# Kernel optimization log

Hardware: AMD Instinct MI355X
Metric: run time of the kernel (lower is better)

The kernel has to match this reference:

```python
import jax, jax.numpy as jnp
import numpy as np

B, N, FIN, E, OUT, NH = 8, 1024, 128, 128, 128, 8
HD = E // NH  # head_dim = 16


def setup_inputs() -> dict:
    key = jax.random.key(0)
    ks = jax.random.split(key, 8)
    s = 0.05
    H = jax.random.normal(ks[0], (B, N, FIN), jnp.float32)
    # binary adjacency (sparse-ish graph), stored dense float as the module expects
    A = (jax.random.uniform(ks[1], (B, N, N)) < 0.05).astype(jnp.float32)
    W_lin = jax.random.normal(ks[2], (FIN, E), jnp.float32) * s
    b_lin = jnp.zeros((E,), jnp.float32)
    # nn.MultiheadAttention packed in-projection (q,k,v) and out-projection
    W_in = jax.random.normal(ks[3], (E, 3 * E), jnp.float32) * s
    b_in = jnp.zeros((3 * E,), jnp.float32)
    W_out = jax.random.normal(ks[4], (E, E), jnp.float32) * s
    b_out = jnp.zeros((E,), jnp.float32)
    W_fin = jax.random.normal(ks[5], (E, OUT), jnp.float32) * s
    b_fin = jnp.zeros((OUT,), jnp.float32)
    return dict(H=H, A=A, W_lin=W_lin, b_lin=b_lin, W_in=W_in, b_in=b_in,
                W_out=W_out, b_out=b_out, W_fin=W_fin, b_fin=b_fin)


def reference(H, A, W_lin, b_lin, W_in, b_in, W_out, b_out, W_fin, b_fin):
    # input projection: Linear(128, embed_dim)
    Hp = H @ W_lin + b_lin                                   # (B,N,E)
    # adjacency-gated attention weights: bmm -> LeakyReLU(0.2) -> *A -> softmax
    s = jnp.einsum('bnd,bmd->bnm', Hp, Hp)                   # (B,N,N)
    s = jnp.where(s >= 0, s, 0.2 * s)
    attn_w = jax.nn.softmax(s * A, axis=-1)                  # (B,N,N)
    # nn.MultiheadAttention self-attention with float attn_mask (ADDED to scores)
    qkv = Hp @ W_in + b_in                                   # (B,N,3E)
    q, k, v = jnp.split(qkv, 3, axis=-1)
    q = q.reshape(B, N, NH, HD)
    k = k.reshape(B, N, NH, HD)
    v = v.reshape(B, N, NH, HD)
    scores = jnp.einsum('bnhd,bmhd->bhnm', q, k) / np.sqrt(HD).astype(np.float32)
    scores = scores + attn_w[:, None]                        # mask broadcast over heads
    p = jax.nn.softmax(scores, axis=-1)                      # (B,NH,N,N)
    o = jnp.einsum('bhnm,bmhd->bnhd', p, v).reshape(B, N, E)
    o = o @ W_out + b_out                                    # MHA out_proj
    # output linear; dropout is identity in eval mode
    return o @ W_fin + b_fin                                 # (B,N,OUT)
```

## Files before the change

kernel.cpp:

```cpp
#include <hip/hip_runtime.h>
#include <hip/hip_bf16.h>


using u16 = unsigned short;
typedef short bf16x8 __attribute__((ext_vector_type(8)));
typedef float f32x4 __attribute__((ext_vector_type(4)));
typedef _Float16 f16;
typedef _Float16 f16x4 __attribute__((ext_vector_type(4)));

#define MFMA16(a, b, c) __builtin_amdgcn_mfma_f32_16x16x16f16(a, b, c, 0, 0, 0)

__device__ __forceinline__ u16 f2b(float f) {
    unsigned u = __float_as_uint(f);
    return (u16)((u + 0x7fffu + ((u >> 16) & 1u)) >> 16);
}
__device__ __forceinline__ float b2f(u16 u) {
    return __uint_as_float(((unsigned)u) << 16);
}

__global__ void prep_hp(const float* __restrict__ H, const float* __restrict__ Wlin,
                        const float* __restrict__ Win,
                        const float* __restrict__ Wout, const float* __restrict__ Wfin,
                        const float* __restrict__ bout, const float* __restrict__ bfin,
                        const float* __restrict__ blin, const float* __restrict__ Aadj,
                        u16* __restrict__ WinTb, u16* __restrict__ WcombTb,
                        float* __restrict__ bcomb, float* __restrict__ rowsum,
                        unsigned char* __restrict__ A8, u16* __restrict__ Hpb) {
    if (blockIdx.x < 64) {
        const int m0 = blockIdx.x * 128;
        const int t = threadIdx.x;
        const int wave = t >> 6, lane = t & 63;
        const int wm = (wave >> 1) * 64, wn = (wave & 1) * 64;
        const int m16 = lane & 15, kq = lane >> 4;
        f32x4 acc[4][4] = {};

#pragma unroll
        for (int kc = 0; kc < 4; ++kc) {
            bf16x8 af[4], bf[4];
#pragma unroll
            for (int i = 0; i < 4; ++i) {
                const float* ap = &H[(long long)(m0 + wm + i * 16 + m16) * 128 + kc * 32 + kq * 8];
                float4 u0 = *(const float4*)ap;
                float4 u1 = *(const float4*)(ap + 4);
                bf16x8 a;
                a[0] = (short)f2b(u0.x); a[1] = (short)f2b(u0.y);
                a[2] = (short)f2b(u0.z); a[3] = (short)f2b(u0.w);
                a[4] = (short)f2b(u1.x); a[5] = (short)f2b(u1.y);
                a[6] = (short)f2b(u1.z); a[7] = (short)f2b(u1.w);
                af[i] = a;
            }
#pragma unroll
            for (int j = 0; j < 4; ++j) {
                const int col = wn + j * 16 + m16;
                const int k0 = kc * 32 + kq * 8;
                bf16x8 bb;
#pragma unroll
                for (int e = 0; e < 8; ++e)
                    bb[e] = (short)f2b(Wlin[(long long)(k0 + e) * 128 + col]);
                bf[j] = bb;
            }
#pragma unroll
            for (int i = 0; i < 4; ++i)
#pragma unroll
                for (int j = 0; j < 4; ++j)
                    acc[i][j] = __builtin_amdgcn_mfma_f32_16x16x32_bf16(af[i], bf[j], acc[i][j], 0, 0, 0);
        }
#pragma unroll
        for (int i = 0; i < 4; ++i) {
#pragma unroll
            for (int r = 0; r < 4; ++r) {
                long long row = m0 + wm + i * 16 + kq * 4 + r;
#pragma unroll
                for (int j = 0; j < 4; ++j) {
                    int col = wn + j * 16 + m16;
                    Hpb[row * 128 + col] = f2b(acc[i][j][r] + blin[col]);
                }
            }
        }
        return;
    }
    int i = (blockIdx.x - 64) * 256 + threadIdx.x;
    if (i >= 81920) {
        int j = i - 81920;
        long long base = (long long)j * 8;
        float4 a0 = *(const float4*)&Aadj[base];
        float4 a1 = *(const float4*)&Aadj[base + 4];
        unsigned long long m = 0;
        m |= (unsigned long long)(a0.x != 0.f) << 0;
        m |= (unsigned long long)(a0.y != 0.f) << 8;
        m |= (unsigned long long)(a0.z != 0.f) << 16;
        m |= (unsigned long long)(a0.w != 0.f) << 24;
        m |= (unsigned long long)(a1.x != 0.f) << 32;
        m |= (unsigned long long)(a1.y != 0.f) << 40;
        m |= (unsigned long long)(a1.z != 0.f) << 48;
        m |= (unsigned long long)(a1.w != 0.f) << 56;
        *(unsigned long long*)&A8[base] = m;
        return;
    }
    if (i < 8192) rowsum[i] = 0.f;
    if (i >= 16384 && i < 65536) {
        int k = i - 16384;
        int r = k / 384, c = k - r * 384;
        WinTb[c * 128 + r] = f2b(Win[k]);
    } else if (i >= 65536) {
        int k = i - 65536;
        int o = k & 127, e = k >> 7;
        float s = 0.f;
        for (int kk = 0; kk < 128; ++kk)
            s = fmaf(Wout[e * 128 + kk], Wfin[kk * 128 + o], s);
        WcombTb[o * 128 + e] = f2b(s);
        if (e == 0) {
            float sb = bfin[o];
            for (int kk = 0; kk < 128; ++kk)
                sb = fmaf(bout[kk], Wfin[kk * 128 + o], sb);
            bcomb[o] = sb;
        }
    }
}

__global__ __launch_bounds__(256)
void mfma_qkvz(const u16* __restrict__ Hpb, const u16* __restrict__ WinTb,
               const float* __restrict__ bin, f16* __restrict__ Cq,
               const unsigned char* __restrict__ G8, u16* __restrict__ EZ,
               float* __restrict__ rowsum) {
    const int blk = blockIdx.x;
    const int t = threadIdx.x;
    const int wave = t >> 6, lane = t & 63;
    const int wm = (wave >> 1) * 64, wn = (wave & 1) * 64;
    const int m16 = lane & 15, kq = lane >> 4;
    f32x4 acc[4][4] = {};

    if (blk < 512) {
        const int b = blk >> 6, mt = (blk >> 3) & 7, nt = blk & 7;
        const u16* Ab = Hpb + (long long)b * 1024 * 128;
        const int m0 = mt * 128, n0 = nt * 128;
#pragma unroll
        for (int kc = 0; kc < 4; ++kc) {
            bf16x8 af[4], bf[4];
#pragma unroll
            for (int i = 0; i < 4; ++i)
                af[i] = *(const bf16x8*)&Ab[(long long)(m0 + wm + i * 16 + m16) * 128 + kc * 32 + kq * 8];
#pragma unroll
            for (int j = 0; j < 4; ++j)
                bf[j] = *(const bf16x8*)&Ab[(long long)(n0 + wn + j * 16 + m16) * 128 + kc * 32 + kq * 8];
#pragma unroll
            for (int i = 0; i < 4; ++i)
#pragma unroll
                for (int j = 0; j < 4; ++j)
                    acc[i][j] = __builtin_amdgcn_mfma_f32_16x16x32_bf16(af[i], bf[j], acc[i][j], 0, 0, 0);
        }
        const long long zb = (long long)b * 1024 * 1024;
#pragma unroll
        for (int i = 0; i < 4; ++i) {
#pragma unroll
            for (int r = 0; r < 4; ++r) {
                int row = m0 + wm + i * 16 + kq * 4 + r;
                float es = 0.f;
#pragma unroll
                for (int j = 0; j < 4; ++j) {
                    int col = n0 + wn + j * 16 + m16;
                    float v = acc[i][j][r];
                    v = v >= 0.f ? v : 0.2f * v;
                    if (!G8[zb + (long long)row * 1024 + col]) v = 0.f;
                    float ev = __expf(v);
                    EZ[zb + (long long)row * 1024 + col] = f2b(ev);
                    es += ev;
                }
#pragma unroll
                for (int off = 1; off < 16; off <<= 1) es += __shfl_xor(es, off);
                if (m16 == 0) atomicAdd(&rowsum[b * 1024 + row], es);
            }
        }
    } else {
        const int q = blk - 512;
        const int mt = q & 63, slab = q >> 6;
        const int m0 = mt * 128;
        const u16* Bslab = WinTb + (long long)slab * 128 * 128;
#pragma unroll
        for (int kc = 0; kc < 4; ++kc) {
            bf16x8 af[4], bf[4];
#pragma unroll
            for (int i = 0; i < 4; ++i)
                af[i] = *(const bf16x8*)&Hpb[(long long)(m0 + wm + i * 16 + m16) * 128 + kc * 32 + kq * 8];
#pragma unroll
            for (int j = 0; j < 4; ++j)
                bf[j] = *(const bf16x8*)&Bslab[(long long)(wn + j * 16 + m16) * 128 + kc * 32 + kq * 8];
#pragma unroll
            for (int i = 0; i < 4; ++i)
#pragma unroll
                for (int j = 0; j < 4; ++j)
                    acc[i][j] = __builtin_amdgcn_mfma_f32_16x16x32_bf16(af[i], bf[j], acc[i][j], 0, 0, 0);
        }
        const float qscale = (slab == 0) ? 0.25f : 1.f;
#pragma unroll
        for (int i = 0; i < 4; ++i) {
#pragma unroll
            for (int r = 0; r < 4; ++r) {
                long long row = m0 + wm + i * 16 + kq * 4 + r;
#pragma unroll
                for (int j = 0; j < 4; ++j) {
                    int col = wn + j * 16 + m16;
                    float v = (acc[i][j][r] + bin[slab * 128 + col]) * qscale;
                    Cq[row * 384 + slab * 128 + col] = (f16)v;
                }
            }
        }
    }
}

__global__ __launch_bounds__(256)
void flash_mfma(const f16* __restrict__ qkv, const u16* __restrict__ ez,
                const float* __restrict__ rowsum, float* __restrict__ o_) {
    const int n0 = blockIdx.x * 64;
    const int b = blockIdx.y;
    const int h0 = blockIdx.z * 2;
    const int t = threadIdx.x;
    const int w = t >> 6, lane = t & 63;
    const int qr16 = lane & 15, quad = lane >> 4;

    __shared__ u16 Ks[64 * 40];
    __shared__ u16 VTs[32 * 76];
    __shared__ u16 AWs[64 * 72];

    const int qrow_l = w * 16 + qr16;
    const long long qrow_g = b * 1024 + n0 + qrow_l;
    const float inv0 = 1.f / rowsum[qrow_g];

    f16x4 qf[2];
#pragma unroll
    for (int hh = 0; hh < 2; ++hh)
        qf[hh] = *(const f16x4*)&qkv[qrow_g * 384 + (h0 + hh) * 16 + quad * 4];

    f32x4 accO[2] = {};
    float lacc[2] = {0.f, 0.f};

    for (int st = 0; st < 16; ++st) {
        const int kb = st * 64;
        __syncthreads();
        {
            const int key = t >> 2, c8 = t & 3;
            *(uint4*)&Ks[key * 40 + c8 * 8] =
                *(const uint4*)&qkv[((long long)(b * 1024 + kb + key)) * 384 + 128 + h0 * 16 + c8 * 8];
            const f16* vsrc = &qkv[((long long)(b * 1024 + kb + key)) * 384 + 256 + h0 * 16 + c8 * 8];
            f16x4 v0 = *(const f16x4*)vsrc;
            f16x4 v1 = *(const f16x4*)(vsrc + 4);
            const int d0 = c8 * 8;
#pragma unroll
            for (int i = 0; i < 4; ++i) {
                VTs[(d0 + i) * 76 + key] = ((const u16*)&v0)[i];
                VTs[(d0 + 4 + i) * 76 + key] = ((const u16*)&v1)[i];
            }
        }
#pragma unroll
        for (int rr = 0; rr < 2; ++rr) {
            int idx = rr * 256 + t;
            int row = idx >> 3, c16 = idx & 7;
            *(uint4*)&AWs[row * 72 + c16 * 8] =
                *(const uint4*)&ez[((long long)(b * 1024 + n0 + row)) * 1024 + kb + c16 * 8];
        }
        __syncthreads();

#pragma unroll 2
        for (int kt = 0; kt < 4; ++kt) {
            ushort4 ue = *(const ushort4*)&AWs[qrow_l * 72 + kt * 16 + quad * 4];
            f32x4 aw0;
            aw0[0] = b2f(ue.x) * inv0; aw0[1] = b2f(ue.y) * inv0;
            aw0[2] = b2f(ue.z) * inv0; aw0[3] = b2f(ue.w) * inv0;
#pragma unroll
            for (int hh = 0; hh < 2; ++hh) {
                f16x4 kf = *(const f16x4*)&Ks[(kt * 16 + qr16) * 40 + hh * 16 + quad * 4];
                f32x4 s4 = MFMA16(kf, qf[hh], aw0);
                float p0 = __expf(s4[0]), p1 = __expf(s4[1]);
                float p2 = __expf(s4[2]), p3 = __expf(s4[3]);
                lacc[hh] += (p0 + p1) + (p2 + p3);
                f16x4 pf;
                pf[0] = (f16)p0; pf[1] = (f16)p1; pf[2] = (f16)p2; pf[3] = (f16)p3;
                f16x4 vf = *(const f16x4*)&VTs[(hh * 16 + qr16) * 76 + kt * 16 + quad * 4];
                accO[hh] = MFMA16(vf, pf, accO[hh]);
            }
        }
    }
#pragma unroll
    for (int hh = 0; hh < 2; ++hh) {
        float l = lacc[hh];
        l += __shfl_xor(l, 16);
        l += __shfl_xor(l, 32);
        float inv = 1.f / l;
        float* orow = o_ + qrow_g * 128 + (h0 + hh) * 16 + quad * 4;
#pragma unroll
        for (int r = 0; r < 4; ++r) orow[r] = accO[hh][r] * inv;
    }
}

__global__ __launch_bounds__(256)
void mfma_out(const float* __restrict__ A, const u16* __restrict__ Bb,
              const float* __restrict__ bias, float* __restrict__ C) {
    const int m0 = blockIdx.x * 128;
    const int t = threadIdx.x;
    const int wave = t >> 6, lane = t & 63;
    const int wm = (wave >> 1) * 64, wn = (wave & 1) * 64;
    const int m16 = lane & 15, kq = lane >> 4;
    f32x4 acc[4][4] = {};

#pragma unroll
    for (int kc = 0; kc < 4; ++kc) {
        bf16x8 af[4], bf[4];
#pragma unroll
        for (int i = 0; i < 4; ++i) {
            const float* ap = &A[(long long)(m0 + wm + i * 16 + m16) * 128 + kc * 32 + kq * 8];
            float4 u0 = *(const float4*)ap;
            float4 u1 = *(const float4*)(ap + 4);
            bf16x8 a;
            a[0] = (short)f2b(u0.x); a[1] = (short)f2b(u0.y);
            a[2] = (short)f2b(u0.z); a[3] = (short)f2b(u0.w);
            a[4] = (short)f2b(u1.x); a[5] = (short)f2b(u1.y);
            a[6] = (short)f2b(u1.z); a[7] = (short)f2b(u1.w);
            af[i] = a;
        }
#pragma unroll
        for (int j = 0; j < 4; ++j)
            bf[j] = *(const bf16x8*)&Bb[(long long)(wn + j * 16 + m16) * 128 + kc * 32 + kq * 8];
#pragma unroll
        for (int i = 0; i < 4; ++i)
#pragma unroll
            for (int j = 0; j < 4; ++j)
                acc[i][j] = __builtin_amdgcn_mfma_f32_16x16x32_bf16(af[i], bf[j], acc[i][j], 0, 0, 0);
    }
#pragma unroll
    for (int i = 0; i < 4; ++i) {
#pragma unroll
        for (int r = 0; r < 4; ++r) {
            long long row = m0 + wm + i * 16 + kq * 4 + r;
#pragma unroll
            for (int j = 0; j < 4; ++j) {
                int col = wn + j * 16 + m16;
                C[row * 128 + col] = acc[i][j][r] + bias[col];
            }
        }
    }
}

extern "C" void kernel_launch(void* const* d_in, const int* in_sizes, int n_in,
                              void* d_out, int out_size, void* d_ws, size_t ws_size,
                              hipStream_t stream) {
    (void)in_sizes; (void)n_in; (void)out_size; (void)ws_size;
    const float* H    = (const float*)d_in[0];
    const float* Aadj = (const float*)d_in[1];
    const float* Wlin = (const float*)d_in[2];
    const float* blin = (const float*)d_in[3];
    const float* Win  = (const float*)d_in[4];
    const float* bin  = (const float*)d_in[5];
    const float* Wout = (const float*)d_in[6];
    const float* bout = (const float*)d_in[7];
    const float* Wfin = (const float*)d_in[8];
    const float* bfin = (const float*)d_in[9];
    float* out = (float*)d_out;
    char* ws = (char*)d_ws;

    u16*   WinTb   = (u16*)(ws + 0);
    u16*   WcombTb = (u16*)(ws + 98304);
    float* bcomb   = (float*)(ws + 131072);
    float* rowsum  = (float*)(ws + 131584);
    u16*   Hpb     = (u16*)(ws + 262144);
    f16*   qkv     = (f16*)(ws + 2359296);
    float* o_      = (float*)(ws + 8650752);
    u16*   ez      = (u16*)(ws + 12845056);
    unsigned char* A8 = (unsigned char*)(ws + 29622272);

    prep_hp<<<4480, 256, 0, stream>>>(H, Wlin, Win, Wout, Wfin, bout, bfin,
                                      blin, Aadj, WinTb, WcombTb, bcomb,
                                      rowsum, A8, Hpb);
    mfma_qkvz<<<704, 256, 0, stream>>>(Hpb, WinTb, bin, qkv, A8, ez, rowsum);
    flash_mfma<<<dim3(16, 8, 4), 256, 0, stream>>>(qkv, ez, rowsum, o_);
    mfma_out<<<64, 256, 0, stream>>>(o_, WcombTb, bcomb, out);
}
```

Before: 160.8 us.

## Fuse four kernels into one persistent megakernel with grid barriers

Merges the prep, QKV/score, flash-attention and output-projection kernels into a single 512-block persistent kernel, with atomic-counter grid barriers between phases. The A-to-byte-mask conversion pass is dropped; the score stage reads the float adjacency directly. The attention output is now stored as bf16 instead of fp32. The aim is to remove launch gaps and the extra pass over A. The cost is software grid-barrier spin latency, and the kernel relies on all 512 blocks being co-resident, which launch_bounds(256,2) is meant to ensure.

```diff
diff --git a/kernel.cpp b/kernel.cpp
--- a/kernel.cpp
+++ b/kernel.cpp
@@ -9,6 +9,7 @@
 typedef _Float16 f16x4 __attribute__((ext_vector_type(4)));
 
 #define MFMA16(a, b, c) __builtin_amdgcn_mfma_f32_16x16x16f16(a, b, c, 0, 0, 0)
+#define MFMAB(a, b, c) __builtin_amdgcn_mfma_f32_16x16x32_bf16(a, b, c, 0, 0, 0)
 
 __device__ __forceinline__ u16 f2b(float f) {
     unsigned u = __float_as_uint(f);
@@ -18,22 +19,42 @@
     return __uint_as_float(((unsigned)u) << 16);
 }
 
-__global__ void prep_hp(const float* __restrict__ H, const float* __restrict__ Wlin,
-                        const float* __restrict__ Win,
-                        const float* __restrict__ Wout, const float* __restrict__ Wfin,
-                        const float* __restrict__ bout, const float* __restrict__ bfin,
-                        const float* __restrict__ blin, const float* __restrict__ Aadj,
-                        u16* __restrict__ WinTb, u16* __restrict__ WcombTb,
-                        float* __restrict__ bcomb, float* __restrict__ rowsum,
-                        unsigned char* __restrict__ A8, u16* __restrict__ Hpb) {
-    if (blockIdx.x < 64) {
-        const int m0 = blockIdx.x * 128;
-        const int t = threadIdx.x;
-        const int wave = t >> 6, lane = t & 63;
-        const int wm = (wave >> 1) * 64, wn = (wave & 1) * 64;
-        const int m16 = lane & 15, kq = lane >> 4;
+__device__ __forceinline__ void gbar(unsigned* __restrict__ c, unsigned nb) {
+    __syncthreads();
+    if (threadIdx.x == 0) {
+        __threadfence();
+        __hip_atomic_fetch_add(c, 1u, __ATOMIC_RELEASE, __HIP_MEMORY_SCOPE_AGENT);
+        while (__hip_atomic_load(c, __ATOMIC_ACQUIRE, __HIP_MEMORY_SCOPE_AGENT) < nb)
+            __builtin_amdgcn_s_sleep(2);
+        __threadfence();
+    }
+    __syncthreads();
+}
+
+__global__ __launch_bounds__(256, 2)
+void gat_mega(const float* __restrict__ H, const float* __restrict__ Aadj,
+              const float* __restrict__ Wlin, const float* __restrict__ blin,
+              const float* __restrict__ Win, const float* __restrict__ bin,
+              const float* __restrict__ Wout, const float* __restrict__ bout,
+              const float* __restrict__ Wfin, const float* __restrict__ bfin,
+              u16* __restrict__ WinTb, u16* __restrict__ WcombTb,
+              float* __restrict__ bcomb, float* __restrict__ rowsum,
+              u16* __restrict__ Hpb, f16* __restrict__ qkv,
+              u16* __restrict__ ez, u16* __restrict__ ob,
+              float* __restrict__ out, unsigned* __restrict__ bars) {
+    __shared__ u16 Ks[64 * 40];
+    __shared__ u16 VTs[32 * 76];
+    __shared__ u16 AWs[64 * 72];
+
+    const int blk = blockIdx.x;
+    const int t = threadIdx.x;
+    const int wave = t >> 6, lane = t & 63;
+    const int wm = (wave >> 1) * 64, wn = (wave & 1) * 64;
+    const int m16 = lane & 15, kq = lane >> 4;
+
+    if (blk < 64) {
+        const int m0 = blk * 128;
         f32x4 acc[4][4] = {};
-
 #pragma unroll
         for (int kc = 0; kc < 4; ++kc) {
             bf16x8 af[4], bf[4];
@@ -63,7 +84,7 @@
             for (int i = 0; i < 4; ++i)
 #pragma unroll
                 for (int j = 0; j < 4; ++j)
-                    acc[i][j] = __builtin_amdgcn_mfma_f32_16x16x32_bf16(af[i], bf[j], acc[i][j], 0, 0, 0);
+                    acc[i][j] = MFMAB(af[i], bf[j], acc[i][j]);
         }
 #pragma unroll
         for (int i = 0; i < 4; ++i) {
@@ -77,121 +98,211 @@
                 }
             }
         }
-        return;
-    }
-    int i = (blockIdx.x - 64) * 256 + threadIdx.x;
-    if (i >= 81920) {
-        int j = i - 81920;
-        long long base = (long long)j * 8;
-        float4 a0 = *(const float4*)&Aadj[base];
-        float4 a1 = *(const float4*)&Aadj[base + 4];
-        unsigned long long m = 0;
-        m |= (unsigned long long)(a0.x != 0.f) << 0;
-        m |= (unsigned long long)(a0.y != 0.f) << 8;
-        m |= (unsigned long long)(a0.z != 0.f) << 16;
-        m |= (unsigned long long)(a0.w != 0.f) << 24;
-        m |= (unsigned long long)(a1.x != 0.f) << 32;
-        m |= (unsigned long long)(a1.y != 0.f) << 40;
-        m |= (unsigned long long)(a1.z != 0.f) << 48;
-        m |= (unsigned long long)(a1.w != 0.f) << 56;
-        *(unsigned long long*)&A8[base] = m;
-        return;
-    }
-    if (i < 8192) rowsum[i] = 0.f;
-    if (i >= 16384 && i < 65536) {
-        int k = i - 16384;
-        int r = k / 384, c = k - r * 384;
-        WinTb[c * 128 + r] = f2b(Win[k]);
-    } else if (i >= 65536) {
-        int k = i - 65536;
-        int o = k & 127, e = k >> 7;
-        float s = 0.f;
-        for (int kk = 0; kk < 128; ++kk)
-            s = fmaf(Wout[e * 128 + kk], Wfin[kk * 128 + o], s);
-        WcombTb[o * 128 + e] = f2b(s);
-        if (e == 0) {
-            float sb = bfin[o];
+    } else {
+        int i = (blk - 64) * 256 + t;
+        if (i < 8192) {
+            rowsum[i] = 0.f;
+        } else if (i < 57344) {
+            int k = i - 8192;
+            int r = k / 384, c = k - r * 384;
+            WinTb[c * 128 + r] = f2b(Win[k]);
+        } else if (i < 73728) {
+            int k = i - 57344;
+            int o = k & 127, e = k >> 7;
+            float s = 0.f;
             for (int kk = 0; kk < 128; ++kk)
-                sb = fmaf(bout[kk], Wfin[kk * 128 + o], sb);
-            bcomb[o] = sb;
-        }
-    }
-}
-
-__global__ __launch_bounds__(256)
-void mfma_qkvz(const u16* __restrict__ Hpb, const u16* __restrict__ WinTb,
-               const float* __restrict__ bin, f16* __restrict__ Cq,
-               const unsigned char* __restrict__ G8, u16* __restrict__ EZ,
-               float* __restrict__ rowsum) {
-    const int blk = blockIdx.x;
-    const int t = threadIdx.x;
-    const int wave = t >> 6, lane = t & 63;
-    const int wm = (wave >> 1) * 64, wn = (wave & 1) * 64;
-    const int m16 = lane & 15, kq = lane >> 4;
-    f32x4 acc[4][4] = {};
-
-    if (blk < 512) {
-        const int b = blk >> 6, mt = (blk >> 3) & 7, nt = blk & 7;
-        const u16* Ab = Hpb + (long long)b * 1024 * 128;
-        const int m0 = mt * 128, n0 = nt * 128;
+                s = fmaf(Wout[e * 128 + kk], Wfin[kk * 128 + o], s);
+            WcombTb[o * 128 + e] = f2b(s);
+            if (e == 0) {
+                float sb = bfin[o];
+                for (int kk = 0; kk < 128; ++kk)
+                    sb = fmaf(bout[kk], Wfin[kk * 128 + o], sb);
+                bcomb[o] = sb;
+            }
+        }
+    }
+    gbar(&bars[0], 512);
+
+    for (int unit = blk; unit < 704; unit += 512) {
+        if (unit < 512) {
+            const int b = unit >> 6, mt = (unit >> 3) & 7, nt = unit & 7;
+            const u16* Ab = Hpb + (long long)b * 1024 * 128;
+            const int m0 = mt * 128, n0 = nt * 128;
+            f32x4 acc[4][4] = {};
+#pragma unroll
+            for (int kc = 0; kc < 4; ++kc) {
+                bf16x8 af[4], bf[4];
+#pragma unroll
+                for (int i = 0; i < 4; ++i)
+                    af[i] = *(const bf16x8*)&Ab[(long long)(m0 + wm + i * 16 + m16) * 128 + kc * 32 + kq * 8];
+#pragma unroll
+                for (int j = 0; j < 4; ++j)
+                    bf[j] = *(const bf16x8*)&Ab[(long long)(n0 + wn + j * 16 + m16) * 128 + kc * 32 + kq * 8];
+#pragma unroll
+                for (int i = 0; i < 4; ++i)
+#pragma unroll
+                    for (int j = 0; j < 4; ++j)
+                        acc[i][j] = MFMAB(af[i], bf[j], acc[i][j]);
+            }
+            const long long zb = (long long)b * 1024 * 1024;
+#pragma unroll
+            for (int i = 0; i < 4; ++i) {
+#pragma unroll
+                for (int r = 0; r < 4; ++r) {
+                    int row = m0 + wm + i * 16 + kq * 4 + r;
+                    float es = 0.f;
+#pragma unroll
+                    for (int j = 0; j < 4; ++j) {
+                        int col = n0 + wn + j * 16 + m16;
+                        float v = acc[i][j][r];
+                        v = v >= 0.f ? v : 0.2f * v;
+                        if (Aadj[zb + (long long)row * 1024 + col] == 0.f) v = 0.f;
+                        float ev = __expf(v);
+                        ez[zb + (long long)row * 1024 + col] = f2b(ev);
+                        es += ev;
+                    }
+#pragma unroll
+                    for (int off = 1; off < 16; off <<= 1) es += __shfl_xor(es, off);
+                    if (m16 == 0) atomicAdd(&rowsum[b * 1024 + row], es);
+                }
+            }
+        } else {
+            const int q = unit - 512;
+            const int mt = q & 63, slab = q >> 6;
+            const int m0 = mt * 128;
+            const u16* Bslab = WinTb + (long long)slab * 128 * 128;
+            f32x4 acc[4][4] = {};
+#pragma unroll
+            for (int kc = 0; kc < 4; ++kc) {
+                bf16x8 af[4], bf[4];
+#pragma unroll
+                for (int i = 0; i < 4; ++i)
+                    af[i] = *(const bf16x8*)&Hpb[(long long)(m0 + wm + i * 16 + m16) * 128 + kc * 32 + kq * 8];
+#pragma unroll
+                for (int j = 0; j < 4; ++j)
+                    bf[j] = *(const bf16x8*)&Bslab[(long long)(wn + j * 16 + m16) * 128 + kc * 32 + kq * 8];
+#pragma unroll
+                for (int i = 0; i < 4; ++i)
+#pragma unroll
+                    for (int j = 0; j < 4; ++j)
+                        acc[i][j] = MFMAB(af[i], bf[j], acc[i][j]);
+            }
+            const float qscale = (slab == 0) ? 0.25f : 1.f;
+#pragma unroll
+            for (int i = 0; i < 4; ++i) {
+#pragma unroll
+                for (int r = 0; r < 4; ++r) {
+                    long long row = m0 + wm + i * 16 + kq * 4 + r;
+#pragma unroll
+                    for (int j = 0; j < 4; ++j) {
+                        int col = wn + j * 16 + m16;
+                        float v = (acc[i][j][r] + bin[slab * 128 + col]) * qscale;
+                        qkv[row * 384 + slab * 128 + col] = (f16)v;
+                    }
+                }
+            }
+        }
+    }
+    gbar(&bars[1], 512);
+
+    {
+        const int n0 = (blk & 15) * 64;
+        const int b = (blk >> 4) & 7;
+        const int h0 = (blk >> 7) * 2;
+        const int qr16 = m16, quad = kq, w = wave;
+
+        const int qrow_l = w * 16 + qr16;
+        const long long qrow_g = b * 1024 + n0 + qrow_l;
+        const float inv0 = 1.f / rowsum[qrow_g];
+
+        f16x4 qf[2];
+#pragma unroll
+        for (int hh = 0; hh < 2; ++hh)
+            qf[hh] = *(const f16x4*)&qkv[qrow_g * 384 + (h0 + hh) * 16 + quad * 4];
+
+        f32x4 accO[2] = {};
+        float lacc[2] = {0.f, 0.f};
+
+        for (int st = 0; st < 16; ++st) {
+            const int kb = st * 64;
+            __syncthreads();
+            {
+                const int key = t >> 2, c8 = t & 3;
+                *(uint4*)&Ks[key * 40 + c8 * 8] =
+                    *(const uint4*)&qkv[((long long)(b * 1024 + kb + key)) * 384 + 128 + h0 * 16 + c8 * 8];
+                const f16* vsrc = &qkv[((long long)(b * 1024 + kb + key)) * 384 + 256 + h0 * 16 + c8 * 8];
+                f16x4 v0 = *(const f16x4*)vsrc;
+                f16x4 v1 = *(const f16x4*)(vsrc + 4);
+                const int d0 = c8 * 8;
+#pragma unroll
+                for (int i = 0; i < 4; ++i) {
+                    VTs[(d0 + i) * 76 + key] = ((const u16*)&v0)[i];
+                    VTs[(d0 + 4 + i) * 76 + key] = ((const u16*)&v1)[i];
+                }
+            }
+#pragma unroll
+            for (int rr = 0; rr < 2; ++rr) {
+                int idx = rr * 256 + t;
+                int row = idx >> 3, c16 = idx & 7;
+                *(uint4*)&AWs[row * 72 + c16 * 8] =
+                    *(const uint4*)&ez[((long long)(b * 1024 + n0 + row)) * 1024 + kb + c16 * 8];
+            }
+            __syncthreads();
+
+#pragma unroll 2
+            for (int kt = 0; kt < 4; ++kt) {
+                ushort4 ue = *(const ushort4*)&AWs[qrow_l * 72 + kt * 16 + quad * 4];
+                f32x4 aw0;
+                aw0[0] = b2f(ue.x) * inv0; aw0[1] = b2f(ue.y) * inv0;
+                aw0[2] = b2f(ue.z) * inv0; aw0[3] = b2f(ue.w) * inv0;
+#pragma unroll
+                for (int hh = 0; hh < 2; ++hh) {
+                    f16x4 kf = *(const f16x4*)&Ks[(kt * 16 + qr16) * 40 + hh * 16 + quad * 4];
+                    f32x4 s4 = MFMA16(kf, qf[hh], aw0);
+                    float p0 = __expf(s4[0]), p1 = __expf(s4[1]);
+                    float p2 = __expf(s4[2]), p3 = __expf(s4[3]);
+                    lacc[hh] += (p0 + p1) + (p2 + p3);
+                    f16x4 pf;
+                    pf[0] = (f16)p0; pf[1] = (f16)p1; pf[2] = (f16)p2; pf[3] = (f16)p3;
+                    f16x4 vf = *(const f16x4*)&VTs[(hh * 16 + qr16) * 76 + kt * 16 + quad * 4];
+                    accO[hh] = MFMA16(vf, pf, accO[hh]);
+                }
+            }
+        }
+#pragma unroll
+        for (int hh = 0; hh < 2; ++hh) {
+            float l = lacc[hh];
+            l += __shfl_xor(l, 16);
+            l += __shfl_xor(l, 32);
+            float inv = 1.f / l;
+            ushort4 st4;
+            st4.x = f2b(accO[hh][0] * inv);
+            st4.y = f2b(accO[hh][1] * inv);
+            st4.z = f2b(accO[hh][2] * inv);
+            st4.w = f2b(accO[hh][3] * inv);
+            *(ushort4*)&ob[qrow_g * 128 + (h0 + hh) * 16 + quad * 4] = st4;
+        }
+    }
+    gbar(&bars[2], 512);
+
+    if (blk < 64) {
+        const int m0 = blk * 128;
+        f32x4 acc[4][4] = {};
 #pragma unroll
         for (int kc = 0; kc < 4; ++kc) {
             bf16x8 af[4], bf[4];
 #pragma unroll
             for (int i = 0; i < 4; ++i)
-                af[i] = *(const bf16x8*)&Ab[(long long)(m0 + wm + i * 16 + m16) * 128 + kc * 32 + kq * 8];
+                af[i] = *(const bf16x8*)&ob[(long long)(m0 + wm + i * 16 + m16) * 128 + kc * 32 + kq * 8];
 #pragma unroll
             for (int j = 0; j < 4; ++j)
-                bf[j] = *(const bf16x8*)&Ab[(long long)(n0 + wn + j * 16 + m16) * 128 + kc * 32 + kq * 8];
+                bf[j] = *(const bf16x8*)&WcombTb[(long long)(wn + j * 16 + m16) * 128 + kc * 32 + kq * 8];
 #pragma unroll
             for (int i = 0; i < 4; ++i)
 #pragma unroll
                 for (int j = 0; j < 4; ++j)
-                    acc[i][j] = __builtin_amdgcn_mfma_f32_16x16x32_bf16(af[i], bf[j], acc[i][j], 0, 0, 0);
-        }
-        const long long zb = (long long)b * 1024 * 1024;
-#pragma unroll
-        for (int i = 0; i < 4; ++i) {
-#pragma unroll
-            for (int r = 0; r < 4; ++r) {
-                int row = m0 + wm + i * 16 + kq * 4 + r;
-                float es = 0.f;
-#pragma unroll
-                for (int j = 0; j < 4; ++j) {
-                    int col = n0 + wn + j * 16 + m16;
-                    float v = acc[i][j][r];
-                    v = v >= 0.f ? v : 0.2f * v;
-                    if (!G8[zb + (long long)row * 1024 + col]) v = 0.f;
-                    float ev = __expf(v);
-                    EZ[zb + (long long)row * 1024 + col] = f2b(ev);
-                    es += ev;
-                }
-#pragma unroll
-                for (int off = 1; off < 16; off <<= 1) es += __shfl_xor(es, off);
-                if (m16 == 0) atomicAdd(&rowsum[b * 1024 + row], es);
-            }
-        }
-    } else {
-        const int q = blk - 512;
-        const int mt = q & 63, slab = q >> 6;
-        const int m0 = mt * 128;
-        const u16* Bslab = WinTb + (long long)slab * 128 * 128;
-#pragma unroll
-        for (int kc = 0; kc < 4; ++kc) {
-            bf16x8 af[4], bf[4];
-#pragma unroll
-            for (int i = 0; i < 4; ++i)
-                af[i] = *(const bf16x8*)&Hpb[(long long)(m0 + wm + i * 16 + m16) * 128 + kc * 32 + kq * 8];
-#pragma unroll
-            for (int j = 0; j < 4; ++j)
-                bf[j] = *(const bf16x8*)&Bslab[(long long)(wn + j * 16 + m16) * 128 + kc * 32 + kq * 8];
-#pragma unroll
-            for (int i = 0; i < 4; ++i)
-#pragma unroll
-                for (int j = 0; j < 4; ++j)
-                    acc[i][j] = __builtin_amdgcn_mfma_f32_16x16x32_bf16(af[i], bf[j], acc[i][j], 0, 0, 0);
-        }
-        const float qscale = (slab == 0) ? 0.25f : 1.f;
+                    acc[i][j] = MFMAB(af[i], bf[j], acc[i][j]);
+        }
 #pragma unroll
         for (int i = 0; i < 4; ++i) {
 #pragma unroll
@@ -200,141 +311,8 @@
 #pragma unroll
                 for (int j = 0; j < 4; ++j) {
                     int col = wn + j * 16 + m16;
-                    float v = (acc[i][j][r] + bin[slab * 128 + col]) * qscale;
-                    Cq[row * 384 + slab * 128 + col] = (f16)v;
-                }
-            }
-        }
-    }
-}
-
-__global__ __launch_bounds__(256)
-void flash_mfma(const f16* __restrict__ qkv, const u16* __restrict__ ez,
-                const float* __restrict__ rowsum, float* __restrict__ o_) {
-    const int n0 = blockIdx.x * 64;
-    const int b = blockIdx.y;
-    const int h0 = blockIdx.z * 2;
-    const int t = threadIdx.x;
-    const int w = t >> 6, lane = t & 63;
-    const int qr16 = lane & 15, quad = lane >> 4;
-
-    __shared__ u16 Ks[64 * 40];
-    __shared__ u16 VTs[32 * 76];
-    __shared__ u16 AWs[64 * 72];
-
-    const int qrow_l = w * 16 + qr16;
-    const long long qrow_g = b * 1024 + n0 + qrow_l;
-    const float inv0 = 1.f / rowsum[qrow_g];
-
-    f16x4 qf[2];
-#pragma unroll
-    for (int hh = 0; hh < 2; ++hh)
-        qf[hh] = *(const f16x4*)&qkv[qrow_g * 384 + (h0 + hh) * 16 + quad * 4];
-
-    f32x4 accO[2] = {};
-    float lacc[2] = {0.f, 0.f};
-
-    for (int st = 0; st < 16; ++st) {
-        const int kb = st * 64;
-        __syncthreads();
-        {
-            const int key = t >> 2, c8 = t & 3;
-            *(uint4*)&Ks[key * 40 + c8 * 8] =
-                *(const uint4*)&qkv[((long long)(b * 1024 + kb + key)) * 384 + 128 + h0 * 16 + c8 * 8];
-            const f16* vsrc = &qkv[((long long)(b * 1024 + kb + key)) * 384 + 256 + h0 * 16 + c8 * 8];
-            f16x4 v0 = *(const f16x4*)vsrc;
-            f16x4 v1 = *(const f16x4*)(vsrc + 4);
-            const int d0 = c8 * 8;
-#pragma unroll
-            for (int i = 0; i < 4; ++i) {
-                VTs[(d0 + i) * 76 + key] = ((const u16*)&v0)[i];
-                VTs[(d0 + 4 + i) * 76 + key] = ((const u16*)&v1)[i];
-            }
-        }
-#pragma unroll
-        for (int rr = 0; rr < 2; ++rr) {
-            int idx = rr * 256 + t;
-            int row = idx >> 3, c16 = idx & 7;
-            *(uint4*)&AWs[row * 72 + c16 * 8] =
-                *(const uint4*)&ez[((long long)(b * 1024 + n0 + row)) * 1024 + kb + c16 * 8];
-        }
-        __syncthreads();
-
-#pragma unroll 2
-        for (int kt = 0; kt < 4; ++kt) {
-            ushort4 ue = *(const ushort4*)&AWs[qrow_l * 72 + kt * 16 + quad * 4];
-            f32x4 aw0;
-            aw0[0] = b2f(ue.x) * inv0; aw0[1] = b2f(ue.y) * inv0;
-            aw0[2] = b2f(ue.z) * inv0; aw0[3] = b2f(ue.w) * inv0;
-#pragma unroll
-            for (int hh = 0; hh < 2; ++hh) {
-                f16x4 kf = *(const f16x4*)&Ks[(kt * 16 + qr16) * 40 + hh * 16 + quad * 4];
-                f32x4 s4 = MFMA16(kf, qf[hh], aw0);
-                float p0 = __expf(s4[0]), p1 = __expf(s4[1]);
-                float p2 = __expf(s4[2]), p3 = __expf(s4[3]);
-                lacc[hh] += (p0 + p1) + (p2 + p3);
-                f16x4 pf;
-                pf[0] = (f16)p0; pf[1] = (f16)p1; pf[2] = (f16)p2; pf[3] = (f16)p3;
-                f16x4 vf = *(const f16x4*)&VTs[(hh * 16 + qr16) * 76 + kt * 16 + quad * 4];
-                accO[hh] = MFMA16(vf, pf, accO[hh]);
-            }
-        }
-    }
-#pragma unroll
-    for (int hh = 0; hh < 2; ++hh) {
-        float l = lacc[hh];
-        l += __shfl_xor(l, 16);
-        l += __shfl_xor(l, 32);
-        float inv = 1.f / l;
-        float* orow = o_ + qrow_g * 128 + (h0 + hh) * 16 + quad * 4;
-#pragma unroll
-        for (int r = 0; r < 4; ++r) orow[r] = accO[hh][r] * inv;
-    }
-}
-
-__global__ __launch_bounds__(256)
-void mfma_out(const float* __restrict__ A, const u16* __restrict__ Bb,
-              const float* __restrict__ bias, float* __restrict__ C) {
-    const int m0 = blockIdx.x * 128;
-    const int t = threadIdx.x;
-    const int wave = t >> 6, lane = t & 63;
-    const int wm = (wave >> 1) * 64, wn = (wave & 1) * 64;
-    const int m16 = lane & 15, kq = lane >> 4;
-    f32x4 acc[4][4] = {};
-
-#pragma unroll
-    for (int kc = 0; kc < 4; ++kc) {
-        bf16x8 af[4], bf[4];
-#pragma unroll
-        for (int i = 0; i < 4; ++i) {
-            const float* ap = &A[(long long)(m0 + wm + i * 16 + m16) * 128 + kc * 32 + kq * 8];
-            float4 u0 = *(const float4*)ap;
-            float4 u1 = *(const float4*)(ap + 4);
-            bf16x8 a;
-            a[0] = (short)f2b(u0.x); a[1] = (short)f2b(u0.y);
-            a[2] = (short)f2b(u0.z); a[3] = (short)f2b(u0.w);
-            a[4] = (short)f2b(u1.x); a[5] = (short)f2b(u1.y);
-            a[6] = (short)f2b(u1.z); a[7] = (short)f2b(u1.w);
-            af[i] = a;
-        }
-#pragma unroll
-        for (int j = 0; j < 4; ++j)
-            bf[j] = *(const bf16x8*)&Bb[(long long)(wn + j * 16 + m16) * 128 + kc * 32 + kq * 8];
-#pragma unroll
-        for (int i = 0; i < 4; ++i)
-#pragma unroll
-            for (int j = 0; j < 4; ++j)
-                acc[i][j] = __builtin_amdgcn_mfma_f32_16x16x32_bf16(af[i], bf[j], acc[i][j], 0, 0, 0);
-    }
-#pragma unroll
-    for (int i = 0; i < 4; ++i) {
-#pragma unroll
-        for (int r = 0; r < 4; ++r) {
-            long long row = m0 + wm + i * 16 + kq * 4 + r;
-#pragma unroll
-            for (int j = 0; j < 4; ++j) {
-                int col = wn + j * 16 + m16;
-                C[row * 128 + col] = acc[i][j][r] + bias[col];
+                    out[row * 128 + col] = acc[i][j][r] + bcomb[col];
+                }
             }
         }
     }
@@ -362,15 +340,13 @@
     float* bcomb   = (float*)(ws + 131072);
     float* rowsum  = (float*)(ws + 131584);
     u16*   Hpb     = (u16*)(ws + 262144);
-    f16*   qkv     = (f16*)(ws + 2359296);
-    float* o_      = (float*)(ws + 8650752);
+    f16*   qkvp    = (f16*)(ws + 2359296);
+    u16*   ob      = (u16*)(ws + 8650752);
     u16*   ez      = (u16*)(ws + 12845056);
-    unsigned char* A8 = (unsigned char*)(ws + 29622272);
-
-    prep_hp<<<4480, 256, 0, stream>>>(H, Wlin, Win, Wout, Wfin, bout, bfin,
-                                      blin, Aadj, WinTb, WcombTb, bcomb,
-                                      rowsum, A8, Hpb);
-    mfma_qkvz<<<704, 256, 0, stream>>>(Hpb, WinTb, bin, qkv, A8, ez, rowsum);
-    flash_mfma<<<dim3(16, 8, 4), 256, 0, stream>>>(qkv, ez, rowsum, o_);
-    mfma_out<<<64, 256, 0, stream>>>(o_, WcombTb, bcomb, out);
-}
+    unsigned* bars = (unsigned*)(ws + 29622272);
+
+    hipMemsetAsync(bars, 0, 16, stream);
+    gat_mega<<<512, 256, 0, stream>>>(H, Aadj, Wlin, blin, Win, bin, Wout,
+                                      bout, Wfin, bfin, WinTb, WcombTb, bcomb,
+                                      rowsum, Hpb, qkvp, ez, ob, out, bars);
+}
```

After: 461.0 us. 2.87x slower.

## Read float adjacency directly in score kernel and store attention output as bf16

Applied to the files above, without the earlier changes.

Drops the separate pass that compressed the float adjacency into a byte mask and instead reads the float adjacency directly inside the score/exp epilogue. This removes a full 32MB read plus an 8MB write and an 8MB reread, and shrinks the prep launch from 4480 to 384 blocks. The attention output is now stored as bf16 rather than fp32, which halves that intermediate and lets the output GEMM load operands without converting them. The trade-off is that the epilogue loads 4-byte strided values instead of bytes, and the output is rounded to bf16 earlier.

```diff
diff --git a/kernel.cpp b/kernel.cpp
--- a/kernel.cpp
+++ b/kernel.cpp
@@ -9,6 +9,7 @@
 typedef _Float16 f16x4 __attribute__((ext_vector_type(4)));
 
 #define MFMA16(a, b, c) __builtin_amdgcn_mfma_f32_16x16x16f16(a, b, c, 0, 0, 0)
+#define MFMAB(a, b, c) __builtin_amdgcn_mfma_f32_16x16x32_bf16(a, b, c, 0, 0, 0)
 
 __device__ __forceinline__ u16 f2b(float f) {
     unsigned u = __float_as_uint(f);
@@ -22,10 +23,10 @@
                         const float* __restrict__ Win,
                         const float* __restrict__ Wout, const float* __restrict__ Wfin,
                         const float* __restrict__ bout, const float* __restrict__ bfin,
-                        const float* __restrict__ blin, const float* __restrict__ Aadj,
+                        const float* __restrict__ blin,
                         u16* __restrict__ WinTb, u16* __restrict__ WcombTb,
                         float* __restrict__ bcomb, float* __restrict__ rowsum,
-                        unsigned char* __restrict__ A8, u16* __restrict__ Hpb) {
+                        u16* __restrict__ Hpb) {
     if (blockIdx.x < 64) {
         const int m0 = blockIdx.x * 128;
         const int t = threadIdx.x;
@@ -63,7 +64,7 @@
             for (int i = 0; i < 4; ++i)
 #pragma unroll
                 for (int j = 0; j < 4; ++j)
-                    acc[i][j] = __builtin_amdgcn_mfma_f32_16x16x32_bf16(af[i], bf[j], acc[i][j], 0, 0, 0);
+                    acc[i][j] = MFMAB(af[i], bf[j], acc[i][j]);
         }
 #pragma unroll
         for (int i = 0; i < 4; ++i) {
@@ -80,23 +81,6 @@
         return;
     }
     int i = (blockIdx.x - 64) * 256 + threadIdx.x;
-    if (i >= 81920) {
-        int j = i - 81920;
-        long long base = (long long)j * 8;
-        float4 a0 = *(const float4*)&Aadj[base];
-        float4 a1 = *(const float4*)&Aadj[base + 4];
-        unsigned long long m = 0;
-        m |= (unsigned long long)(a0.x != 0.f) << 0;
-        m |= (unsigned long long)(a0.y != 0.f) << 8;
-        m |= (unsigned long long)(a0.z != 0.f) << 16;
-        m |= (unsigned long long)(a0.w != 0.f) << 24;
-        m |= (unsigned long long)(a1.x != 0.f) << 32;
-        m |= (unsigned long long)(a1.y != 0.f) << 40;
-        m |= (unsigned long long)(a1.z != 0.f) << 48;
-        m |= (unsigned long long)(a1.w != 0.f) << 56;
-        *(unsigned long long*)&A8[base] = m;
-        return;
-    }
     if (i < 8192) rowsum[i] = 0.f;
     if (i >= 16384 && i < 65536) {
         int k = i - 16384;
@@ -121,7 +105,7 @@
 __global__ __launch_bounds__(256)
 void mfma_qkvz(const u16* __restrict__ Hpb, const u16* __restrict__ WinTb,
                const float* __restrict__ bin, f16* __restrict__ Cq,
-               const unsigned char* __restrict__ G8, u16* __restrict__ EZ,
+               const float* __restrict__ Aadj, u16* __restrict__ EZ,
                float* __restrict__ rowsum) {
     const int blk = blockIdx.x;
     const int t = threadIdx.x;
@@ -147,7 +131,7 @@
             for (int i = 0; i < 4; ++i)
 #pragma unroll
                 for (int j = 0; j < 4; ++j)
-                    acc[i][j] = __builtin_amdgcn_mfma_f32_16x16x32_bf16(af[i], bf[j], acc[i][j], 0, 0, 0);
+                    acc[i][j] = MFMAB(af[i], bf[j], acc[i][j]);
         }
         const long long zb = (long long)b * 1024 * 1024;
 #pragma unroll
@@ -161,7 +145,7 @@
                     int col = n0 + wn + j * 16 + m16;
                     float v = acc[i][j][r];
                     v = v >= 0.f ? v : 0.2f * v;
-                    if (!G8[zb + (long long)row * 1024 + col]) v = 0.f;
+                    if (Aadj[zb + (long long)row * 1024 + col] == 0.f) v = 0.f;
                     float ev = __expf(v);
                     EZ[zb + (long long)row * 1024 + col] = f2b(ev);
                     es += ev;
@@ -189,7 +173,7 @@
             for (int i = 0; i < 4; ++i)
 #pragma unroll
                 for (int j = 0; j < 4; ++j)
-                    acc[i][j] = __builtin_amdgcn_mfma_f32_16x16x32_bf16(af[i], bf[j], acc[i][j], 0, 0, 0);
+                    acc[i][j] = MFMAB(af[i], bf[j], acc[i][j]);
         }
         const float qscale = (slab == 0) ? 0.25f : 1.f;
 #pragma unroll
@@ -210,7 +194,7 @@
 
 __global__ __launch_bounds__(256)
 void flash_mfma(const f16* __restrict__ qkv, const u16* __restrict__ ez,
-                const float* __restrict__ rowsum, float* __restrict__ o_) {
+                const float* __restrict__ rowsum, u16* __restrict__ ob) {
     const int n0 = blockIdx.x * 64;
     const int b = blockIdx.y;
     const int h0 = blockIdx.z * 2;
@@ -286,14 +270,17 @@
         l += __shfl_xor(l, 16);
         l += __shfl_xor(l, 32);
         float inv = 1.f / l;
-        float* orow = o_ + qrow_g * 128 + (h0 + hh) * 16 + quad * 4;
-#pragma unroll
-        for (int r = 0; r < 4; ++r) orow[r] = accO[hh][r] * inv;
+        ushort4 st4;
+        st4.x = f2b(accO[hh][0] * inv);
+        st4.y = f2b(accO[hh][1] * inv);
+        st4.z = f2b(accO[hh][2] * inv);
+        st4.w = f2b(accO[hh][3] * inv);
+        *(ushort4*)&ob[qrow_g * 128 + (h0 + hh) * 16 + quad * 4] = st4;
     }
 }
 
 __global__ __launch_bounds__(256)
-void mfma_out(const float* __restrict__ A, const u16* __restrict__ Bb,
+void mfma_out(const u16* __restrict__ A, const u16* __restrict__ Bb,
               const float* __restrict__ bias, float* __restrict__ C) {
     const int m0 = blockIdx.x * 128;
     const int t = threadIdx.x;
@@ -306,17 +293,8 @@
     for (int kc = 0; kc < 4; ++kc) {
         bf16x8 af[4], bf[4];
 #pragma unroll
-        for (int i = 0; i < 4; ++i) {
-            const float* ap = &A[(long long)(m0 + wm + i * 16 + m16) * 128 + kc * 32 + kq * 8];
-            float4 u0 = *(const float4*)ap;
-            float4 u1 = *(const float4*)(ap + 4);
-            bf16x8 a;
-            a[0] = (short)f2b(u0.x); a[1] = (short)f2b(u0.y);
-            a[2] = (short)f2b(u0.z); a[3] = (short)f2b(u0.w);
-            a[4] = (short)f2b(u1.x); a[5] = (short)f2b(u1.y);
-            a[6] = (short)f2b(u1.z); a[7] = (short)f2b(u1.w);
-            af[i] = a;
-        }
+        for (int i = 0; i < 4; ++i)
+            af[i] = *(const bf16x8*)&A[(long long)(m0 + wm + i * 16 + m16) * 128 + kc * 32 + kq * 8];
 #pragma unroll
         for (int j = 0; j < 4; ++j)
             bf[j] = *(const bf16x8*)&Bb[(long long)(wn + j * 16 + m16) * 128 + kc * 32 + kq * 8];
@@ -324,7 +302,7 @@
         for (int i = 0; i < 4; ++i)
 #pragma unroll
             for (int j = 0; j < 4; ++j)
-                acc[i][j] = __builtin_amdgcn_mfma_f32_16x16x32_bf16(af[i], bf[j], acc[i][j], 0, 0, 0);
+                acc[i][j] = MFMAB(af[i], bf[j], acc[i][j]);
     }
 #pragma unroll
     for (int i = 0; i < 4; ++i) {
@@ -363,14 +341,12 @@
     float* rowsum  = (float*)(ws + 131584);
     u16*   Hpb     = (u16*)(ws + 262144);
     f16*   qkv     = (f16*)(ws + 2359296);
-    float* o_      = (float*)(ws + 8650752);
+    u16*   ob      = (u16*)(ws + 8650752);
     u16*   ez      = (u16*)(ws + 12845056);
-    unsigned char* A8 = (unsigned char*)(ws + 29622272);
-
-    prep_hp<<<4480, 256, 0, stream>>>(H, Wlin, Win, Wout, Wfin, bout, bfin,
-                                      blin, Aadj, WinTb, WcombTb, bcomb,
-                                      rowsum, A8, Hpb);
-    mfma_qkvz<<<704, 256, 0, stream>>>(Hpb, WinTb, bin, qkv, A8, ez, rowsum);
-    flash_mfma<<<dim3(16, 8, 4), 256, 0, stream>>>(qkv, ez, rowsum, o_);
-    mfma_out<<<64, 256, 0, stream>>>(o_, WcombTb, bcomb, out);
-}
+
+    prep_hp<<<384, 256, 0, stream>>>(H, Wlin, Win, Wout, Wfin, bout, bfin,
+                                     blin, WinTb, WcombTb, bcomb, rowsum, Hpb);
+    mfma_qkvz<<<704, 256, 0, stream>>>(Hpb, WinTb, bin, qkv, Aadj, ez, rowsum);
+    flash_mfma<<<dim3(16, 8, 4), 256, 0, stream>>>(qkv, ez, rowsum, ob);
+    mfma_out<<<64, 256, 0, stream>>>(ob, WcombTb, bcomb, out);
+}
```

After: 159.8 us. About the same (-0.7%).
